# Kernel optimization log

Hardware: AMD Instinct MI355X
Metric: run time of the kernel (lower is better)

## Reference

```python
import jax, jax.numpy as jnp
import numpy as np

B, S, DIM = 1, 2048, 4096
N_HEADS, N_KV_HEADS = 32, 8
HEAD_DIM = DIM // N_HEADS            # 128
N_REP = N_HEADS // N_KV_HEADS        # 4
Q_SIZE = N_HEADS * HEAD_DIM          # 4096
KV_SIZE = N_KV_HEADS * HEAD_DIM      # 1024


def setup_inputs() -> dict:
    key = jax.random.key(0)
    ks = jax.random.split(key, 5)
    x = jax.random.normal(ks[0], (B, S, DIM), dtype=jnp.float32)
    # RoPE tables: freqs_cis[s, j] = exp(i * s * theta_j), theta_j = 10000^(-2j/head_dim)
    theta = 10000.0 ** (-jnp.arange(0, HEAD_DIM, 2, dtype=jnp.float32) / HEAD_DIM)
    ang = jnp.arange(S, dtype=jnp.float32)[:, None] * theta[None, :]  # [S, HEAD_DIM//2]
    freqs_cos = jnp.cos(ang)
    freqs_sin = jnp.sin(ang)
    # causal additive mask [1,1,S,S]
    causal = jnp.tril(jnp.ones((S, S), dtype=bool))
    mask = jnp.where(causal, 0.0, -1e9).astype(jnp.float32)[None, None]
    wqkv = jax.random.normal(ks[1], (Q_SIZE + 2 * KV_SIZE, DIM), dtype=jnp.float32) * (DIM ** -0.5)
    wo = jax.random.normal(ks[2], (DIM, Q_SIZE), dtype=jnp.float32) * (Q_SIZE ** -0.5)
    return {"x": x, "freqs_cos": freqs_cos, "freqs_sin": freqs_sin, "mask": mask,
            "wqkv": wqkv, "wo": wo}


def _apply_rope(t, cos, sin):
    # t: [B, S, H, D]; cos/sin: [S, D//2]  (complex multiply on (even, odd) pairs)
    b, s, h, d = t.shape
    tp = t.reshape(b, s, h, d // 2, 2)
    t0, t1 = tp[..., 0], tp[..., 1]
    c = cos[None, :, None, :]
    sn = sin[None, :, None, :]
    out = jnp.stack([t0 * c - t1 * sn, t0 * sn + t1 * c], axis=-1)
    return out.reshape(b, s, h, d)


def reference(x, freqs_cos, freqs_sin, mask, wqkv, wo):
    bsz, seqlen, _ = x.shape
    qkv = jnp.einsum('bsd,od->bso', x, wqkv)  # fused QKV projection
    xq = qkv[..., :Q_SIZE].reshape(bsz, seqlen, N_HEADS, HEAD_DIM)
    xk = qkv[..., Q_SIZE:Q_SIZE + KV_SIZE].reshape(bsz, seqlen, N_KV_HEADS, HEAD_DIM)
    xv = qkv[..., Q_SIZE + KV_SIZE:].reshape(bsz, seqlen, N_KV_HEADS, HEAD_DIM)
    # rotary embedding on q, k
    xq = _apply_rope(xq, freqs_cos, freqs_sin)
    xk = _apply_rope(xk, freqs_cos, freqs_sin)
    # cache insertion (prefill: cache == current k/v), layout [B, KVH, S, D]
    cache_k = jnp.swapaxes(xk, 1, 2)
    cache_v = jnp.swapaxes(xv, 1, 2)
    # GQA repeat_kv -> [B, H, S, D]
    keys = jnp.repeat(cache_k, N_REP, axis=1)
    values = jnp.repeat(cache_v, N_REP, axis=1)
    # scores: einsum 'ijkl,ikml->ikjm' with xq [b,s,h,d], keys [b,h,t,d] -> [b,h,s,t]
    scores = jnp.einsum('bshd,bhtd->bhst', xq, keys) / jnp.sqrt(jnp.float32(HEAD_DIM))
    scores = scores + mask
    scores = jax.nn.softmax(scores.astype(jnp.float32), axis=-1).astype(xq.dtype)
    out = jnp.einsum('bhst,bhtd->bhsd', scores, values)  # [B, H, S, D]
    out = jnp.swapaxes(out, 1, 2).reshape(bsz, seqlen, Q_SIZE)
    return jnp.einsum('bso,do->bsd', out, wo)
```

## Files before the change

### kernel.cpp

```cpp
#include <hip/hip_runtime.h>
#include <hip/hip_bf16.h>
#include <cstdint>
#include <cstddef>


typedef __attribute__((ext_vector_type(4)))  float    f32x4;
typedef __attribute__((ext_vector_type(16))) float    f32x16;
typedef __attribute__((ext_vector_type(8)))  __bf16   bf16x8;
typedef __attribute__((ext_vector_type(4)))  __bf16   bf16x4;
typedef __attribute__((ext_vector_type(2)))  __bf16   bf16x2;
typedef __attribute__((ext_vector_type(4)))  uint32_t u32x4;

typedef const __attribute__((address_space(1))) void* gaddr_t;
typedef __attribute__((address_space(3))) void*       laddr_t;

#define S_LEN   2048
#define DIM_    4096
#define NHEADS  32
#define NKV     8
#define HD      128
#define QKV_LD  6144
#define KOFF    4096
#define VOFF    5120

#define EXP2F(x) __builtin_amdgcn_exp2f(x)

__global__ void cvt_f32_bf16(const float* __restrict__ in, __bf16* __restrict__ out, int n4) {
  int idx = blockIdx.x * blockDim.x + threadIdx.x;
  int stride = gridDim.x * blockDim.x;
  for (int i = idx; i < n4; i += stride) {
    float4 v = reinterpret_cast<const float4*>(in)[i];
    bf16x4 o;
    o[0] = (__bf16)v.x; o[1] = (__bf16)v.y; o[2] = (__bf16)v.z; o[3] = (__bf16)v.w;
    reinterpret_cast<bf16x4*>(out)[i] = o;
  }
}

__global__ void rope_kernel(__bf16* __restrict__ qkv, const float* __restrict__ fc,
                            const float* __restrict__ fs) {
  int tid = blockIdx.x * 256 + threadIdx.x;
  int i = tid & 63;
  int t = tid >> 6;
  int h = t % 40;
  int s = t / 40;
  int col = (h < NHEADS) ? (h * HD + 2 * i) : (KOFF + (h - NHEADS) * HD + 2 * i);
  size_t off = (size_t)s * QKV_LD + col;
  float c = fc[s * 64 + i], sn = fs[s * 64 + i];
  bf16x2 v = *reinterpret_cast<bf16x2*>(&qkv[off]);
  float t0 = (float)v[0], t1 = (float)v[1];
  bf16x2 o;
  o[0] = (__bf16)(t0 * c - t1 * sn);
  o[1] = (__bf16)(t0 * sn + t1 * c);
  *reinterpret_cast<bf16x2*>(&qkv[off]) = o;
}

__device__ __forceinline__ void stage64(const __bf16* __restrict__ P, int ld, int row0,
                                        int kt, char* dst, int tid) {
  int r = tid >> 3, g = tid & 7;
  const __bf16* src = P + (size_t)(row0 + r) * ld + kt * 64 + ((g ^ (r & 7)) * 8);
  __builtin_amdgcn_global_load_lds((gaddr_t)src,
      (laddr_t)(dst + (tid & ~63) * 16), 16, 0, 0);
}

template <int MW, int NW, int KH, int NST, bool VM>
__device__ __forceinline__ void phase32(const __bf16* __restrict__ Ab,
                                        const __bf16* __restrict__ Bb,
                                        f32x16 (&acc)[MW][NW],
                                        int wm, int wn, int l31, int hi, int tid,
                                        const __bf16* __restrict__ SP, int sld,
                                        int srow0, char* sdst, int kt, bool st) {
  bf16x8 af[MW][2], bfr[NW][2];
#pragma unroll
  for (int mi = 0; mi < MW; ++mi) {
    int R = wm * (MW * 32) + mi * 32 + l31;
#pragma unroll
    for (int k2 = 0; k2 < 2; ++k2)
      af[mi][k2] = *reinterpret_cast<const bf16x8*>(
          (const char*)Ab + R * 128 + (((KH * 4 + k2 * 2 + hi) ^ (R & 7)) * 16));
  }
#pragma unroll
  for (int ni = 0; ni < NW; ++ni) {
    int R = wn * (NW * 32) + ni * 32 + l31;
#pragma unroll
    for (int k2 = 0; k2 < 2; ++k2)
      bfr[ni][k2] = *reinterpret_cast<const bf16x8*>(
          (const char*)Bb + R * 128 + (((KH * 4 + k2 * 2 + hi) ^ (R & 7)) * 16));
  }
  if (st) {
#pragma unroll
    for (int h = 0; h < NST; ++h)
      stage64(SP, sld, srow0 + h * 64, kt, sdst + h * 8192, tid);
  }
  __builtin_amdgcn_s_barrier();
  asm volatile("s_waitcnt lgkmcnt(0)" ::: "memory");
  __builtin_amdgcn_sched_barrier(0);
  __builtin_amdgcn_s_setprio(1);
#pragma unroll
  for (int k2 = 0; k2 < 2; ++k2)
#pragma unroll
    for (int mi = 0; mi < MW; ++mi)
#pragma unroll
      for (int ni = 0; ni < NW; ++ni)
        acc[mi][ni] = __builtin_amdgcn_mfma_f32_32x32x16_bf16(af[mi][k2], bfr[ni][k2],
                                                              acc[mi][ni], 0, 0, 0);
  __builtin_amdgcn_s_setprio(0);
  if (VM) asm volatile("s_waitcnt vmcnt(0)" ::: "memory");
  __builtin_amdgcn_s_barrier();
}

template <int BM, int BN, int MB, int NPX, typename OutT>
__global__ __launch_bounds__(512, 1) void gemm32(const __bf16* __restrict__ A,
                                                 const __bf16* __restrict__ B,
                                                 OutT* __restrict__ C, int K,
                                                 int lda, int ldb, int ldc) {
  constexpr int MW = BM / 64;
  constexpr int NW = BN / 128;
  constexpr int AST = BM / 64, BST = BN / 64;
  __shared__ __align__(16) __bf16 As[2][BM * 64];
  __shared__ __align__(16) __bf16 Bs[2][BN * 64];
  const int tid = threadIdx.x;
  const int lane = tid & 63, l31 = lane & 31, hi = lane >> 5, w = tid >> 6;
  const int wm = w >> 2, wn = w & 3;
  const int bid = blockIdx.x, xcd = bid & 7, lid = bid >> 3;
  const int m0 = (lid % MB) * BM;
  const int n0 = (xcd * NPX + lid / MB) * BN;

  f32x16 acc[MW][NW] = {};

#pragma unroll
  for (int h = 0; h < AST; ++h) stage64(A, lda, m0 + h * 64, 0, (char*)As[0] + h * 8192, tid);
#pragma unroll
  for (int h = 0; h < BST; ++h) stage64(B, ldb, n0 + h * 64, 0, (char*)Bs[0] + h * 8192, tid);
  asm volatile("s_waitcnt vmcnt(0)" ::: "memory");
  __builtin_amdgcn_s_barrier();

  const int ntiles = K >> 6;
  for (int t = 0; t < ntiles; ++t) {
    const int cur = t & 1;
    const __bf16* Ab = As[cur];
    const __bf16* Bb = Bs[cur];
    char* dA = (char*)As[1 - cur];
    char* dB = (char*)Bs[1 - cur];
    const bool st = (t + 1 < ntiles);
    phase32<MW, NW, 0, AST, false>(Ab, Bb, acc, wm, wn, l31, hi, tid,
                                   A, lda, m0, dA, t + 1, st);
    phase32<MW, NW, 1, BST, true >(Ab, Bb, acc, wm, wn, l31, hi, tid,
                                   B, ldb, n0, dB, t + 1, st);
  }

#pragma unroll
  for (int mi = 0; mi < MW; ++mi)
#pragma unroll
    for (int ni = 0; ni < NW; ++ni)
#pragma unroll
      for (int e = 0; e < 16; ++e) {
        int row = m0 + wm * (MW * 32) + mi * 32 + (e & 3) + 8 * (e >> 2) + 4 * hi;
        int col = n0 + wn * (NW * 32) + ni * 32 + l31;
        C[(size_t)row * ldc + col] = (OutT)acc[mi][ni][e];
      }
}

__device__ inline uint32_t pack2(float a, float b) {
  bf16x2 t; t[0] = (__bf16)a; t[1] = (__bf16)b;
  return __builtin_bit_cast(uint32_t, t);
}

__global__ __launch_bounds__(256, 2) void attn_kernel(const __bf16* __restrict__ qkv,
                                                      __bf16* __restrict__ out) {
  __shared__ __align__(16) __bf16 Ks[2][64 * 128];
  __shared__ __align__(16) __bf16 Vt[2][128][72];
  const int tid = threadIdx.x;
  const int lane = tid & 63, l31 = lane & 31, hi = lane >> 5, wq = tid >> 6;
  const int head = blockIdx.x & 31;
  const int pr = blockIdx.x >> 5;
  const int kvh = head >> 2;
  const float sc2 = 0.08838834764831845f * 1.44269504089f;

  bf16x8 vr[2][2];

  auto stage_k = [&](int tt, int buf) {
#pragma unroll
    for (int i = 0; i < 4; ++i) {
      int c = i * 256 + tid;
      int r = c >> 4, g = c & 15;
      const __bf16* gk = qkv + (size_t)(tt * 64 + r) * QKV_LD + KOFF + kvh * HD + ((g ^ (r & 7)) * 8);
      __builtin_amdgcn_global_load_lds((gaddr_t)gk,
          (laddr_t)((char*)Ks[buf] + (tid & ~63) * 16 + i * 4096), 16, 0, 0);
    }
  };
  auto load_v = [&](int tt) {
#pragma unroll
    for (int i = 0; i < 2; ++i) {
      int task = i * 256 + tid;
      int p = task >> 4, cg = task & 15;
      const __bf16* vp = qkv + (size_t)(tt * 64 + 2 * p) * QKV_LD + VOFF + kvh * HD + cg * 8;
      vr[i][0] = *reinterpret_cast<const bf16x8*>(vp);
      vr[i][1] = *reinterpret_cast<const bf16x8*>(vp + QKV_LD);
    }
  };
  auto write_v = [&](int buf) {
#pragma unroll
    for (int i = 0; i < 2; ++i) {
      int task = i * 256 + tid;
      int p = task >> 4, cg = task & 15;
#pragma unroll
      for (int e0 = 0; e0 < 8; ++e0) {
        int e = e0 ^ (lane & 7);
        bf16x2 pkv; pkv[0] = vr[i][0][e]; pkv[1] = vr[i][1][e];
        *reinterpret_cast<bf16x2*>(&Vt[buf][cg * 8 + e][2 * p]) = pkv;
      }
    }
  };

  for (int pass = 0; pass < 2; ++pass) {
    const int qt = pass ? (15 - pr) : pr;
    const int q0 = qt * 128;
    const int nt = 2 * qt + 2;
    const int qr = q0 + wq * 32 + l31;

    bf16x8 qf[8];
    {
      const __bf16* qp = qkv + (size_t)qr * QKV_LD + head * HD + hi * 8;
#pragma unroll
      for (int ks = 0; ks < 8; ++ks) qf[ks] = *reinterpret_cast<const bf16x8*>(qp + ks * 16);
    }
    f32x16 o[4] = {};
    float m_run = -3e38f, l_run = 0.f;

    __syncthreads();
    stage_k(0, 0); load_v(0); write_v(0);

    for (int t = 0; t < nt; ++t) {
      const int cur = t & 1;
      __syncthreads();
      if (t + 1 < nt) { stage_k(t + 1, 1 - cur); load_v(t + 1); }

      f32x16 st[2];
#pragma unroll
      for (int sub = 0; sub < 2; ++sub) {
        f32x16 acc = {};
        int r = sub * 32 + l31;
#pragma unroll
        for (int ks = 0; ks < 8; ++ks) {
          int g = (ks * 2 + hi) ^ (r & 7);
          bf16x8 kf = *reinterpret_cast<const bf16x8*>((char*)Ks[cur] + r * 256 + g * 16);
          acc = __builtin_amdgcn_mfma_f32_32x32x16_bf16(kf, qf[ks], acc, 0, 0, 0);
        }
        st[sub] = acc;
      }
#pragma unroll
      for (int sub = 0; sub < 2; ++sub)
#pragma unroll
        for (int e = 0; e < 16; ++e) st[sub][e] *= sc2;
      if (t >= nt - 2) {
        const int kv0 = t * 64;
#pragma unroll
        for (int sub = 0; sub < 2; ++sub)
#pragma unroll
          for (int e = 0; e < 16; ++e) {
            int kvg = kv0 + sub * 32 + (e & 3) + 8 * (e >> 2) + 4 * hi;
            if (kvg > qr) st[sub][e] = -1e30f;
          }
      }
      float pm = st[0][0];
#pragma unroll
      for (int e = 1; e < 16; ++e) pm = fmaxf(pm, st[0][e]);
#pragma unroll
      for (int e = 0; e < 16; ++e) pm = fmaxf(pm, st[1][e]);
      pm = fmaxf(pm, __shfl_xor(pm, 32));
      if (!__all(pm - m_run <= 8.f)) {
        float mn = fmaxf(m_run, pm);
        float fsc = EXP2F(m_run - mn);
        m_run = mn;
        l_run *= fsc;
#pragma unroll
        for (int dt = 0; dt < 4; ++dt)
#pragma unroll
          for (int e = 0; e < 16; ++e) o[dt][e] *= fsc;
      }
      float rs = 0.f;
#pragma unroll
      for (int sub = 0; sub < 2; ++sub)
#pragma unroll
        for (int e = 0; e < 16; ++e) {
          float p = EXP2F(st[sub][e] - m_run);
          st[sub][e] = p;
          rs += p;
        }
      rs += __shfl_xor(rs, 32);
      l_run += rs;

      uint32_t pk[16];
#pragma unroll
      for (int sub = 0; sub < 2; ++sub)
#pragma unroll
        for (int i = 0; i < 8; ++i)
          pk[sub * 8 + i] = pack2(st[sub][2 * i], st[sub][2 * i + 1]);
      uint32_t rv[8];
#pragma unroll
      for (int m = 0; m < 8; ++m) {
        int base = 4 * (m >> 1) + (m & 1);
        uint32_t snd = hi ? pk[base] : pk[base + 2];
        rv[m] = __shfl_xor(snd, 32);
      }
      bf16x8 pf[4];
#pragma unroll
      for (int tt = 0; tt < 4; ++tt) {
        u32x4 w;
        w[0] = hi ? rv[2 * tt]     : pk[4 * tt];
        w[1] = hi ? rv[2 * tt + 1] : pk[4 * tt + 1];
        w[2] = hi ? pk[4 * tt + 2] : rv[2 * tt];
        w[3] = hi ? pk[4 * tt + 3] : rv[2 * tt + 1];
        pf[tt] = __builtin_bit_cast(bf16x8, w);
      }
#pragma unroll
      for (int dt = 0; dt < 4; ++dt) {
        int dr = dt * 32 + l31;
#pragma unroll
        for (int tt = 0; tt < 4; ++tt) {
          bf16x8 vf = *reinterpret_cast<const bf16x8*>((char*)&Vt[cur][0][0] + dr * 144 + tt * 32 + hi * 16);
          o[dt] = __builtin_amdgcn_mfma_f32_32x32x16_bf16(vf, pf[tt], o[dt], 0, 0, 0);
        }
      }
      if (t + 1 < nt) write_v(1 - cur);
    }

    float inv = 1.f / l_run;
    __bf16* scr = &Ks[0][0] + wq * 1280;
    const int qq = lane >> 1, part = lane & 1;
#pragma unroll
    for (int dt = 0; dt < 4; ++dt) {
      __syncthreads();
#pragma unroll
      for (int i = 0; i < 8; ++i) {
        int d0 = (2 * i & 3) + 8 * (i >> 1) + 4 * hi;
        bf16x2 prr;
        prr[0] = (__bf16)(o[dt][2 * i] * inv);
        prr[1] = (__bf16)(o[dt][2 * i + 1] * inv);
        *reinterpret_cast<bf16x2*>(scr + l31 * 40 + d0) = prr;
      }
      __syncthreads();
      bf16x8 r0 = *reinterpret_cast<const bf16x8*>(scr + qq * 40 + part * 16);
      bf16x8 r1 = *reinterpret_cast<const bf16x8*>(scr + qq * 40 + part * 16 + 8);
      __bf16* op = out + (size_t)(q0 + wq * 32 + qq) * DIM_ + head * HD + dt * 32 + part * 16;
      *reinterpret_cast<bf16x8*>(op) = r0;
      *reinterpret_cast<bf16x8*>(op + 8) = r1;
    }
  }
}

extern "C" void kernel_launch(void* const* d_in, const int* in_sizes, int n_in,
                              void* d_out, int out_size, void* d_ws, size_t ws_size,
                              hipStream_t stream) {
  (void)in_sizes; (void)n_in; (void)out_size; (void)ws_size;
  const float* x    = (const float*)d_in[0];
  const float* fc   = (const float*)d_in[1];
  const float* fs   = (const float*)d_in[2];
  const float* wqkv = (const float*)d_in[4];
  const float* wo   = (const float*)d_in[5];
  float* out = (float*)d_out;

  char* ws = (char*)d_ws;
  __bf16* xb    = (__bf16*)(ws);
  __bf16* wqkvb = (__bf16*)(ws + 16777216);
  __bf16* wob   = (__bf16*)(ws + 67108864);
  __bf16* qkv   = (__bf16*)(ws + 100663296);
  __bf16* attnO = xb;

  cvt_f32_bf16<<<2048, 256, 0, stream>>>(x,    xb,    (S_LEN * DIM_) / 4);
  cvt_f32_bf16<<<2048, 256, 0, stream>>>(wqkv, wqkvb, (6144 * DIM_) / 4);
  cvt_f32_bf16<<<2048, 256, 0, stream>>>(wo,   wob,   (DIM_ * DIM_) / 4);

  gemm32<256, 256, 8, 3, __bf16><<<192, 512, 0, stream>>>(xb, wqkvb, qkv, DIM_, DIM_, DIM_, QKV_LD);

  rope_kernel<<<(S_LEN * 40 * 64) / 256, 256, 0, stream>>>(qkv, fc, fs);

  attn_kernel<<<256, 256, 0, stream>>>(qkv, attnO);

  gemm32<128, 256, 16, 2, float><<<256, 512, 0, stream>>>(attnO, wob, out, DIM_, DIM_, DIM_, DIM_);
}
```

Before: 369.7 us.

## Fuse fp32-to-bf16 weight conversion into GEMM B loads; split attention passes into blocks

```diff
diff --git a/kernel.cpp b/kernel.cpp
--- a/kernel.cpp
+++ b/kernel.cpp
@@ -54,98 +54,149 @@
   *reinterpret_cast<bf16x2*>(&qkv[off]) = o;
 }
 
-__device__ __forceinline__ void stage64(const __bf16* __restrict__ P, int ld, int row0,
-                                        int kt, char* dst, int tid) {
+__device__ __forceinline__ void stgA(const __bf16* __restrict__ P, int ld, int row0,
+                                     int kt, char* dst, int tid) {
   int r = tid >> 3, g = tid & 7;
   const __bf16* src = P + (size_t)(row0 + r) * ld + kt * 64 + ((g ^ (r & 7)) * 8);
   __builtin_amdgcn_global_load_lds((gaddr_t)src,
       (laddr_t)(dst + (tid & ~63) * 16), 16, 0, 0);
 }
 
-template <int MW, int NW, int KH, int NST, bool VM>
-__device__ __forceinline__ void phase32(const __bf16* __restrict__ Ab,
-                                        const __bf16* __restrict__ Bb,
-                                        f32x16 (&acc)[MW][NW],
-                                        int wm, int wn, int l31, int hi, int tid,
-                                        const __bf16* __restrict__ SP, int sld,
-                                        int srow0, char* sdst, int kt, bool st) {
-  bf16x8 af[MW][2], bfr[NW][2];
-#pragma unroll
-  for (int mi = 0; mi < MW; ++mi) {
-    int R = wm * (MW * 32) + mi * 32 + l31;
-#pragma unroll
-    for (int k2 = 0; k2 < 2; ++k2)
-      af[mi][k2] = *reinterpret_cast<const bf16x8*>(
-          (const char*)Ab + R * 128 + (((KH * 4 + k2 * 2 + hi) ^ (R & 7)) * 16));
-  }
-#pragma unroll
-  for (int ni = 0; ni < NW; ++ni) {
-    int R = wn * (NW * 32) + ni * 32 + l31;
-#pragma unroll
-    for (int k2 = 0; k2 < 2; ++k2)
-      bfr[ni][k2] = *reinterpret_cast<const bf16x8*>(
-          (const char*)Bb + R * 128 + (((KH * 4 + k2 * 2 + hi) ^ (R & 7)) * 16));
-  }
-  if (st) {
-#pragma unroll
-    for (int h = 0; h < NST; ++h)
-      stage64(SP, sld, srow0 + h * 64, kt, sdst + h * 8192, tid);
-  }
-  __builtin_amdgcn_s_barrier();
-  asm volatile("s_waitcnt lgkmcnt(0)" ::: "memory");
-  __builtin_amdgcn_sched_barrier(0);
-  __builtin_amdgcn_s_setprio(1);
-#pragma unroll
-  for (int k2 = 0; k2 < 2; ++k2)
-#pragma unroll
-    for (int mi = 0; mi < MW; ++mi)
-#pragma unroll
-      for (int ni = 0; ni < NW; ++ni)
-        acc[mi][ni] = __builtin_amdgcn_mfma_f32_32x32x16_bf16(af[mi][k2], bfr[ni][k2],
-                                                              acc[mi][ni], 0, 0, 0);
-  __builtin_amdgcn_s_setprio(0);
-  if (VM) asm volatile("s_waitcnt vmcnt(0)" ::: "memory");
-  __builtin_amdgcn_s_barrier();
-}
-
-template <int BM, int BN, int MB, int NPX, typename OutT>
-__global__ __launch_bounds__(512, 1) void gemm32(const __bf16* __restrict__ A,
-                                                 const __bf16* __restrict__ B,
-                                                 OutT* __restrict__ C, int K,
-                                                 int lda, int ldb, int ldc) {
+template <int BM, int MB, int NPX, typename OutT>
+__global__ __launch_bounds__(512) void gemmF(const __bf16* __restrict__ A,
+                                             const float* __restrict__ Bf,
+                                             OutT* __restrict__ C, int K,
+                                             int lda, int ldb, int ldc) {
   constexpr int MW = BM / 64;
-  constexpr int NW = BN / 128;
-  constexpr int AST = BM / 64, BST = BN / 64;
+  constexpr int NW = 2;
+  constexpr int AST = BM / 64;
   __shared__ __align__(16) __bf16 As[2][BM * 64];
-  __shared__ __align__(16) __bf16 Bs[2][BN * 64];
+  __shared__ __align__(16) __bf16 Bs[2][256 * 64];
   const int tid = threadIdx.x;
   const int lane = tid & 63, l31 = lane & 31, hi = lane >> 5, w = tid >> 6;
   const int wm = w >> 2, wn = w & 3;
   const int bid = blockIdx.x, xcd = bid & 7, lid = bid >> 3;
   const int m0 = (lid % MB) * BM;
-  const int n0 = (xcd * NPX + lid / MB) * BN;
+  const int n0 = (xcd * NPX + lid / MB) * 256;
+  const int rB = tid >> 3, gB = tid & 7;
+  const int gSw = (gB ^ (rB & 7)) * 8;
 
   f32x16 acc[MW][NW] = {};
-
-#pragma unroll
-  for (int h = 0; h < AST; ++h) stage64(A, lda, m0 + h * 64, 0, (char*)As[0] + h * 8192, tid);
-#pragma unroll
-  for (int h = 0; h < BST; ++h) stage64(B, ldb, n0 + h * 64, 0, (char*)Bs[0] + h * 8192, tid);
+  f32x4 br[4][2];
+
+  auto loadB = [&](int kt) {
+#pragma unroll
+    for (int h = 0; h < 4; ++h) {
+      const float* s = Bf + (size_t)(n0 + h * 64 + rB) * ldb + kt * 64 + gSw;
+      br[h][0] = *reinterpret_cast<const f32x4*>(s);
+      br[h][1] = *reinterpret_cast<const f32x4*>(s + 4);
+    }
+  };
+  auto writeB = [&](char* dB) {
+#pragma unroll
+    for (int h = 0; h < 4; ++h) {
+      bf16x8 v;
+#pragma unroll
+      for (int j = 0; j < 4; ++j) {
+        v[j]     = (__bf16)br[h][0][j];
+        v[4 + j] = (__bf16)br[h][1][j];
+      }
+      *reinterpret_cast<bf16x8*>(dB + h * 8192 + tid * 16) = v;
+    }
+  };
+
+#pragma unroll
+  for (int h = 0; h < AST; ++h) stgA(A, lda, m0 + h * 64, 0, (char*)As[0] + h * 8192, tid);
+  loadB(0);
   asm volatile("s_waitcnt vmcnt(0)" ::: "memory");
+  writeB((char*)Bs[0]);
+  asm volatile("s_waitcnt lgkmcnt(0)" ::: "memory");
   __builtin_amdgcn_s_barrier();
 
-  const int ntiles = K >> 6;
-  for (int t = 0; t < ntiles; ++t) {
+  const int nt = K >> 6;
+  for (int t = 0; t < nt; ++t) {
     const int cur = t & 1;
     const __bf16* Ab = As[cur];
     const __bf16* Bb = Bs[cur];
     char* dA = (char*)As[1 - cur];
     char* dB = (char*)Bs[1 - cur];
-    const bool st = (t + 1 < ntiles);
-    phase32<MW, NW, 0, AST, false>(Ab, Bb, acc, wm, wn, l31, hi, tid,
-                                   A, lda, m0, dA, t + 1, st);
-    phase32<MW, NW, 1, BST, true >(Ab, Bb, acc, wm, wn, l31, hi, tid,
-                                   B, ldb, n0, dB, t + 1, st);
+    const bool st = (t + 1 < nt);
+
+    {
+      bf16x8 af[MW][2], bfr[NW][2];
+#pragma unroll
+      for (int mi = 0; mi < MW; ++mi) {
+        int R = wm * (MW * 32) + mi * 32 + l31;
+#pragma unroll
+        for (int k2 = 0; k2 < 2; ++k2)
+          af[mi][k2] = *reinterpret_cast<const bf16x8*>(
+              (const char*)Ab + R * 128 + (((k2 * 2 + hi) ^ (R & 7)) * 16));
+      }
+#pragma unroll
+      for (int ni = 0; ni < NW; ++ni) {
+        int R = wn * 64 + ni * 32 + l31;
+#pragma unroll
+        for (int k2 = 0; k2 < 2; ++k2)
+          bfr[ni][k2] = *reinterpret_cast<const bf16x8*>(
+              (const char*)Bb + R * 128 + (((k2 * 2 + hi) ^ (R & 7)) * 16));
+      }
+      if (st) {
+#pragma unroll
+        for (int h = 0; h < AST; ++h) stgA(A, lda, m0 + h * 64, t + 1, dA + h * 8192, tid);
+        loadB(t + 1);
+      }
+      __builtin_amdgcn_s_barrier();
+      asm volatile("s_waitcnt lgkmcnt(0)" ::: "memory");
+      __builtin_amdgcn_sched_barrier(0);
+      __builtin_amdgcn_s_setprio(1);
+#pragma unroll
+      for (int k2 = 0; k2 < 2; ++k2)
+#pragma unroll
+        for (int mi = 0; mi < MW; ++mi)
+#pragma unroll
+          for (int ni = 0; ni < NW; ++ni)
+            acc[mi][ni] = __builtin_amdgcn_mfma_f32_32x32x16_bf16(af[mi][k2], bfr[ni][k2],
+                                                                  acc[mi][ni], 0, 0, 0);
+      __builtin_amdgcn_s_setprio(0);
+      __builtin_amdgcn_s_barrier();
+    }
+    {
+      bf16x8 af[MW][2], bfr[NW][2];
+#pragma unroll
+      for (int mi = 0; mi < MW; ++mi) {
+        int R = wm * (MW * 32) + mi * 32 + l31;
+#pragma unroll
+        for (int k2 = 0; k2 < 2; ++k2)
+          af[mi][k2] = *reinterpret_cast<const bf16x8*>(
+              (const char*)Ab + R * 128 + (((4 + k2 * 2 + hi) ^ (R & 7)) * 16));
+      }
+#pragma unroll
+      for (int ni = 0; ni < NW; ++ni) {
+        int R = wn * 64 + ni * 32 + l31;
+#pragma unroll
+        for (int k2 = 0; k2 < 2; ++k2)
+          bfr[ni][k2] = *reinterpret_cast<const bf16x8*>(
+              (const char*)Bb + R * 128 + (((4 + k2 * 2 + hi) ^ (R & 7)) * 16));
+      }
+      if (st) {
+        asm volatile("s_waitcnt vmcnt(0)" ::: "memory");
+        writeB(dB);
+      }
+      __builtin_amdgcn_s_barrier();
+      asm volatile("s_waitcnt lgkmcnt(0)" ::: "memory");
+      __builtin_amdgcn_sched_barrier(0);
+      __builtin_amdgcn_s_setprio(1);
+#pragma unroll
+      for (int k2 = 0; k2 < 2; ++k2)
+#pragma unroll
+        for (int mi = 0; mi < MW; ++mi)
+#pragma unroll
+          for (int ni = 0; ni < NW; ++ni)
+            acc[mi][ni] = __builtin_amdgcn_mfma_f32_32x32x16_bf16(af[mi][k2], bfr[ni][k2],
+                                                                  acc[mi][ni], 0, 0, 0);
+      __builtin_amdgcn_s_setprio(0);
+      __builtin_amdgcn_s_barrier();
+    }
   }
 
 #pragma unroll
@@ -155,7 +206,7 @@
 #pragma unroll
       for (int e = 0; e < 16; ++e) {
         int row = m0 + wm * (MW * 32) + mi * 32 + (e & 3) + 8 * (e >> 2) + 4 * hi;
-        int col = n0 + wn * (NW * 32) + ni * 32 + l31;
+        int col = n0 + wn * 64 + ni * 32 + l31;
         C[(size_t)row * ldc + col] = (OutT)acc[mi][ni][e];
       }
 }
@@ -172,9 +223,13 @@
   const int tid = threadIdx.x;
   const int lane = tid & 63, l31 = lane & 31, hi = lane >> 5, wq = tid >> 6;
   const int head = blockIdx.x & 31;
-  const int pr = blockIdx.x >> 5;
+  const int g = blockIdx.x >> 5;
+  const int qt = (g < 8) ? (15 - g) : (g - 8);
+  const int q0 = qt * 128;
+  const int nt = 2 * qt + 2;
   const int kvh = head >> 2;
   const float sc2 = 0.08838834764831845f * 1.44269504089f;
+  const int qr = q0 + wq * 32 + l31;
 
   bf16x8 vr[2][2];
 
@@ -182,8 +237,8 @@
 #pragma unroll
     for (int i = 0; i < 4; ++i) {
       int c = i * 256 + tid;
-      int r = c >> 4, g = c & 15;
-      const __bf16* gk = qkv + (size_t)(tt * 64 + r) * QKV_LD + KOFF + kvh * HD + ((g ^ (r & 7)) * 8);
+      int r = c >> 4, gg = c & 15;
+      const __bf16* gk = qkv + (size_t)(tt * 64 + r) * QKV_LD + KOFF + kvh * HD + ((gg ^ (r & 7)) * 8);
       __builtin_amdgcn_global_load_lds((gaddr_t)gk,
           (laddr_t)((char*)Ks[buf] + (tid & ~63) * 16 + i * 4096), 16, 0, 0);
     }
@@ -212,140 +267,132 @@
     }
   };
 
-  for (int pass = 0; pass < 2; ++pass) {
-    const int qt = pass ? (15 - pr) : pr;
-    const int q0 = qt * 128;
-    const int nt = 2 * qt + 2;
-    const int qr = q0 + wq * 32 + l31;
-
-    bf16x8 qf[8];
-    {
-      const __bf16* qp = qkv + (size_t)qr * QKV_LD + head * HD + hi * 8;
-#pragma unroll
-      for (int ks = 0; ks < 8; ++ks) qf[ks] = *reinterpret_cast<const bf16x8*>(qp + ks * 16);
-    }
-    f32x16 o[4] = {};
-    float m_run = -3e38f, l_run = 0.f;
-
+  bf16x8 qf[8];
+  {
+    const __bf16* qp = qkv + (size_t)qr * QKV_LD + head * HD + hi * 8;
+#pragma unroll
+    for (int ks = 0; ks < 8; ++ks) qf[ks] = *reinterpret_cast<const bf16x8*>(qp + ks * 16);
+  }
+  f32x16 o[4] = {};
+  float m_run = -3e38f, l_run = 0.f;
+
+  stage_k(0, 0); load_v(0); write_v(0);
+
+  for (int t = 0; t < nt; ++t) {
+    const int cur = t & 1;
     __syncthreads();
-    stage_k(0, 0); load_v(0); write_v(0);
-
-    for (int t = 0; t < nt; ++t) {
-      const int cur = t & 1;
-      __syncthreads();
-      if (t + 1 < nt) { stage_k(t + 1, 1 - cur); load_v(t + 1); }
-
-      f32x16 st[2];
-#pragma unroll
-      for (int sub = 0; sub < 2; ++sub) {
-        f32x16 acc = {};
-        int r = sub * 32 + l31;
-#pragma unroll
-        for (int ks = 0; ks < 8; ++ks) {
-          int g = (ks * 2 + hi) ^ (r & 7);
-          bf16x8 kf = *reinterpret_cast<const bf16x8*>((char*)Ks[cur] + r * 256 + g * 16);
-          acc = __builtin_amdgcn_mfma_f32_32x32x16_bf16(kf, qf[ks], acc, 0, 0, 0);
+    if (t + 1 < nt) { stage_k(t + 1, 1 - cur); load_v(t + 1); }
+
+    f32x16 st[2];
+#pragma unroll
+    for (int sub = 0; sub < 2; ++sub) {
+      f32x16 acc = {};
+      int r = sub * 32 + l31;
+#pragma unroll
+      for (int ks = 0; ks < 8; ++ks) {
+        int gg = (ks * 2 + hi) ^ (r & 7);
+        bf16x8 kf = *reinterpret_cast<const bf16x8*>((char*)Ks[cur] + r * 256 + gg * 16);
+        acc = __builtin_amdgcn_mfma_f32_32x32x16_bf16(kf, qf[ks], acc, 0, 0, 0);
+      }
+      st[sub] = acc;
+    }
+#pragma unroll
+    for (int sub = 0; sub < 2; ++sub)
+#pragma unroll
+      for (int e = 0; e < 16; ++e) st[sub][e] *= sc2;
+    if (t >= nt - 2) {
+      const int kv0 = t * 64;
+#pragma unroll
+      for (int sub = 0; sub < 2; ++sub)
+#pragma unroll
+        for (int e = 0; e < 16; ++e) {
+          int kvg = kv0 + sub * 32 + (e & 3) + 8 * (e >> 2) + 4 * hi;
+          if (kvg > qr) st[sub][e] = -1e30f;
         }
-        st[sub] = acc;
-      }
-#pragma unroll
-      for (int sub = 0; sub < 2; ++sub)
-#pragma unroll
-        for (int e = 0; e < 16; ++e) st[sub][e] *= sc2;
-      if (t >= nt - 2) {
-        const int kv0 = t * 64;
-#pragma unroll
-        for (int sub = 0; sub < 2; ++sub)
-#pragma unroll
-          for (int e = 0; e < 16; ++e) {
-            int kvg = kv0 + sub * 32 + (e & 3) + 8 * (e >> 2) + 4 * hi;
-            if (kvg > qr) st[sub][e] = -1e30f;
-          }
-      }
-      float pm = st[0][0];
-#pragma unroll
-      for (int e = 1; e < 16; ++e) pm = fmaxf(pm, st[0][e]);
-#pragma unroll
-      for (int e = 0; e < 16; ++e) pm = fmaxf(pm, st[1][e]);
-      pm = fmaxf(pm, __shfl_xor(pm, 32));
-      if (!__all(pm - m_run <= 8.f)) {
-        float mn = fmaxf(m_run, pm);
-        float fsc = EXP2F(m_run - mn);
-        m_run = mn;
-        l_run *= fsc;
-#pragma unroll
-        for (int dt = 0; dt < 4; ++dt)
-#pragma unroll
-          for (int e = 0; e < 16; ++e) o[dt][e] *= fsc;
-      }
-      float rs = 0.f;
-#pragma unroll
-      for (int sub = 0; sub < 2; ++sub)
-#pragma unroll
-        for (int e = 0; e < 16; ++e) {
-          float p = EXP2F(st[sub][e] - m_run);
-          st[sub][e] = p;
-          rs += p;
-        }
-      rs += __shfl_xor(rs, 32);
-      l_run += rs;
-
-      uint32_t pk[16];
-#pragma unroll
-      for (int sub = 0; sub < 2; ++sub)
-#pragma unroll
-        for (int i = 0; i < 8; ++i)
-          pk[sub * 8 + i] = pack2(st[sub][2 * i], st[sub][2 * i + 1]);
-      uint32_t rv[8];
-#pragma unroll
-      for (int m = 0; m < 8; ++m) {
-        int base = 4 * (m >> 1) + (m & 1);
-        uint32_t snd = hi ? pk[base] : pk[base + 2];
-        rv[m] = __shfl_xor(snd, 32);
-      }
-      bf16x8 pf[4];
+    }
+    float pm = st[0][0];
+#pragma unroll
+    for (int e = 1; e < 16; ++e) pm = fmaxf(pm, st[0][e]);
+#pragma unroll
+    for (int e = 0; e < 16; ++e) pm = fmaxf(pm, st[1][e]);
+    pm = fmaxf(pm, __shfl_xor(pm, 32));
+    if (!__all(pm - m_run <= 8.f)) {
+      float mn = fmaxf(m_run, pm);
+      float fsc = EXP2F(m_run - mn);
+      m_run = mn;
+      l_run *= fsc;
+#pragma unroll
+      for (int dt = 0; dt < 4; ++dt)
+#pragma unroll
+        for (int e = 0; e < 16; ++e) o[dt][e] *= fsc;
+    }
+    float rs = 0.f;
+#pragma unroll
+    for (int sub = 0; sub < 2; ++sub)
+#pragma unroll
+      for (int e = 0; e < 16; ++e) {
+        float p = EXP2F(st[sub][e] - m_run);
+        st[sub][e] = p;
+        rs += p;
+      }
+    rs += __shfl_xor(rs, 32);
+    l_run += rs;
+
+    uint32_t pk[16];
+#pragma unroll
+    for (int sub = 0; sub < 2; ++sub)
+#pragma unroll
+      for (int i = 0; i < 8; ++i)
+        pk[sub * 8 + i] = pack2(st[sub][2 * i], st[sub][2 * i + 1]);
+    uint32_t rv[8];
+#pragma unroll
+    for (int m = 0; m < 8; ++m) {
+      int base = 4 * (m >> 1) + (m & 1);
+      uint32_t snd = hi ? pk[base] : pk[base + 2];
+      rv[m] = __shfl_xor(snd, 32);
+    }
+    bf16x8 pf[4];
+#pragma unroll
+    for (int tt = 0; tt < 4; ++tt) {
+      u32x4 wv;
+      wv[0] = hi ? rv[2 * tt]     : pk[4 * tt];
+      wv[1] = hi ? rv[2 * tt + 1] : pk[4 * tt + 1];
+      wv[2] = hi ? pk[4 * tt + 2] : rv[2 * tt];
+      wv[3] = hi ? pk[4 * tt + 3] : rv[2 * tt + 1];
+      pf[tt] = __builtin_bit_cast(bf16x8, wv);
+    }
+#pragma unroll
+    for (int dt = 0; dt < 4; ++dt) {
+      int dr = dt * 32 + l31;
 #pragma unroll
       for (int tt = 0; tt < 4; ++tt) {
-        u32x4 w;
-        w[0] = hi ? rv[2 * tt]     : pk[4 * tt];
-        w[1] = hi ? rv[2 * tt + 1] : pk[4 * tt + 1];
-        w[2] = hi ? pk[4 * tt + 2] : rv[2 * tt];
-        w[3] = hi ? pk[4 * tt + 3] : rv[2 * tt + 1];
-        pf[tt] = __builtin_bit_cast(bf16x8, w);
-      }
-#pragma unroll
-      for (int dt = 0; dt < 4; ++dt) {
-        int dr = dt * 32 + l31;
-#pragma unroll
-        for (int tt = 0; tt < 4; ++tt) {
-          bf16x8 vf = *reinterpret_cast<const bf16x8*>((char*)&Vt[cur][0][0] + dr * 144 + tt * 32 + hi * 16);
-          o[dt] = __builtin_amdgcn_mfma_f32_32x32x16_bf16(vf, pf[tt], o[dt], 0, 0, 0);
-        }
-      }
-      if (t + 1 < nt) write_v(1 - cur);
-    }
-
-    float inv = 1.f / l_run;
-    __bf16* scr = &Ks[0][0] + wq * 1280;
-    const int qq = lane >> 1, part = lane & 1;
-#pragma unroll
-    for (int dt = 0; dt < 4; ++dt) {
-      __syncthreads();
-#pragma unroll
-      for (int i = 0; i < 8; ++i) {
-        int d0 = (2 * i & 3) + 8 * (i >> 1) + 4 * hi;
-        bf16x2 prr;
-        prr[0] = (__bf16)(o[dt][2 * i] * inv);
-        prr[1] = (__bf16)(o[dt][2 * i + 1] * inv);
-        *reinterpret_cast<bf16x2*>(scr + l31 * 40 + d0) = prr;
-      }
-      __syncthreads();
-      bf16x8 r0 = *reinterpret_cast<const bf16x8*>(scr + qq * 40 + part * 16);
-      bf16x8 r1 = *reinterpret_cast<const bf16x8*>(scr + qq * 40 + part * 16 + 8);
-      __bf16* op = out + (size_t)(q0 + wq * 32 + qq) * DIM_ + head * HD + dt * 32 + part * 16;
-      *reinterpret_cast<bf16x8*>(op) = r0;
-      *reinterpret_cast<bf16x8*>(op + 8) = r1;
-    }
+        bf16x8 vf = *reinterpret_cast<const bf16x8*>((char*)&Vt[cur][0][0] + dr * 144 + tt * 32 + hi * 16);
+        o[dt] = __builtin_amdgcn_mfma_f32_32x32x16_bf16(vf, pf[tt], o[dt], 0, 0, 0);
+      }
+    }
+    if (t + 1 < nt) write_v(1 - cur);
+  }
+
+  float inv = 1.f / l_run;
+  __bf16* scr = &Ks[0][0] + wq * 1280;
+  const int qq = lane >> 1, part = lane & 1;
+#pragma unroll
+  for (int dt = 0; dt < 4; ++dt) {
+    __syncthreads();
+#pragma unroll
+    for (int i = 0; i < 8; ++i) {
+      int d0 = (2 * i & 3) + 8 * (i >> 1) + 4 * hi;
+      bf16x2 prr;
+      prr[0] = (__bf16)(o[dt][2 * i] * inv);
+      prr[1] = (__bf16)(o[dt][2 * i + 1] * inv);
+      *reinterpret_cast<bf16x2*>(scr + l31 * 40 + d0) = prr;
+    }
+    __syncthreads();
+    bf16x8 r0 = *reinterpret_cast<const bf16x8*>(scr + qq * 40 + part * 16);
+    bf16x8 r1 = *reinterpret_cast<const bf16x8*>(scr + qq * 40 + part * 16 + 8);
+    __bf16* op = out + (size_t)(q0 + wq * 32 + qq) * DIM_ + head * HD + dt * 32 + part * 16;
+    *reinterpret_cast<bf16x8*>(op) = r0;
+    *reinterpret_cast<bf16x8*>(op + 8) = r1;
   }
 }
 
@@ -361,21 +408,17 @@
   float* out = (float*)d_out;
 
   char* ws = (char*)d_ws;
-  __bf16* xb    = (__bf16*)(ws);
-  __bf16* wqkvb = (__bf16*)(ws + 16777216);
-  __bf16* wob   = (__bf16*)(ws + 67108864);
-  __bf16* qkv   = (__bf16*)(ws + 100663296);
+  __bf16* xb  = (__bf16*)(ws);
+  __bf16* qkv = (__bf16*)(ws + 16777216);
   __bf16* attnO = xb;
 
-  cvt_f32_bf16<<<2048, 256, 0, stream>>>(x,    xb,    (S_LEN * DIM_) / 4);
-  cvt_f32_bf16<<<2048, 256, 0, stream>>>(wqkv, wqkvb, (6144 * DIM_) / 4);
-  cvt_f32_bf16<<<2048, 256, 0, stream>>>(wo,   wob,   (DIM_ * DIM_) / 4);
-
-  gemm32<256, 256, 8, 3, __bf16><<<192, 512, 0, stream>>>(xb, wqkvb, qkv, DIM_, DIM_, DIM_, QKV_LD);
+  cvt_f32_bf16<<<2048, 256, 0, stream>>>(x, xb, (S_LEN * DIM_) / 4);
+
+  gemmF<256, 8, 3, __bf16><<<192, 512, 0, stream>>>(xb, wqkv, qkv, DIM_, DIM_, DIM_, QKV_LD);
 
   rope_kernel<<<(S_LEN * 40 * 64) / 256, 256, 0, stream>>>(qkv, fc, fs);
 
-  attn_kernel<<<256, 256, 0, stream>>>(qkv, attnO);
-
-  gemm32<128, 256, 16, 2, float><<<256, 512, 0, stream>>>(attnO, wob, out, DIM_, DIM_, DIM_, DIM_);
-}
+  attn_kernel<<<512, 256, 0, stream>>>(qkv, attnO);
+
+  gemmF<128, 16, 2, float><<<256, 512, 0, stream>>>(attnO, wo, out, DIM_, DIM_, DIM_, DIM_);
+}
```

After: 426.2 us. 1.15x slower.
